# Kernel tuning notes

Hardware: AMD Instinct MI355X
Metric: run time of the kernel (lower is better)

## Reference

```python
import jax, jax.numpy as jnp
import numpy as np

B, S, D = 8, 8192, 512
E, DFF = 16, 512
CAPACITY = 2


def setup_inputs() -> dict:
    key = jax.random.key(0)
    ks = jax.random.split(key, 4)
    x = jax.random.normal(ks[0], (B, S, D), dtype=jnp.float32)
    gate_weight = jax.random.normal(ks[1], (D, E), dtype=jnp.float32) * 0.006
    w1 = jax.random.normal(ks[2], (E, D, DFF), dtype=jnp.float32) * 0.02
    b1 = jnp.zeros((E, DFF), dtype=jnp.float32)
    w2 = jax.random.normal(ks[3], (E, DFF, D), dtype=jnp.float32) * 0.02
    b2 = jnp.zeros((E, D), dtype=jnp.float32)
    return {"x": x, "gate_weight": gate_weight, "w1": w1, "b1": b1, "w2": w2, "b2": b2}


def reference(x, gate_weight, w1, b1, w2, b2):
    Bx, Sx, Dx = x.shape
    num_experts = gate_weight.shape[1]
    k = Sx // num_experts * CAPACITY  # tokens per expert (capacity limit)

    # Router: softmax over experts, then each expert picks its top-k tokens.
    logits = jnp.einsum('bsd,de->bse', x, gate_weight)
    affinity = jax.nn.softmax(logits, axis=-1).transpose(0, 2, 1)  # [b, e, s]
    gating, index = jax.lax.top_k(affinity, k)  # [b, e, k] each

    # Dispatch: gather selected tokens per expert (== one-hot einsum in torch).
    x_in = jnp.take_along_axis(x[:, None, :, :], index[..., None], axis=2)  # [b, e, k, d]

    # Per-expert MLP (grouped GEMM over expert axis).
    h = jax.nn.gelu(jnp.einsum('bekd,edh->bekh', x_in, w1) + b1[None, :, None, :])
    x_e = jnp.einsum('bekh,ehd->bekd', h, w2) + b2[None, :, None, :]

    # Combine: weight by gate prob and scatter-add back to token positions.
    weighted = gating[..., None] * x_e  # [b, e, k, d]
    out = jnp.zeros_like(x)
    idx_flat = index.reshape(Bx, num_experts * k)
    vals_flat = weighted.reshape(Bx, num_experts * k, Dx)
    out = out.at[jnp.arange(Bx)[:, None], idx_flat].add(vals_flat)
    return out
```

## Files before the change

kernel.cpp:

```cpp
#include <hip/hip_runtime.h>
#include <hip/hip_bf16.h>

typedef __attribute__((ext_vector_type(8))) short short8;
typedef __attribute__((ext_vector_type(4))) float floatx4;
typedef __attribute__((ext_vector_type(4))) unsigned short ushort4_t;

#define B_    8
#define S_    8192
#define D_    512
#define E_    16
#define DFF_  512
#define KROW_ 1024

__device__ __forceinline__ float bf2f(unsigned short u) {
    return __uint_as_float(((unsigned int)u) << 16);
}
__device__ __forceinline__ unsigned short f2bf(float f) {
    unsigned int u = __float_as_uint(f);
    u += 0x7FFFu + ((u >> 16) & 1u);
    return (unsigned short)(u >> 16);
}
__device__ __forceinline__ float gelu_tanh(float v) {
    const float t = 1.5957691216057308f * v * fmaf(0.044715f, v * v, 1.0f);
    return v * __builtin_amdgcn_rcpf(1.0f + __expf(-t));
}

#define GLD16(g, l) __builtin_amdgcn_global_load_lds( \
    (const __attribute__((address_space(1))) void*)(g), \
    (__attribute__((address_space(3))) void*)(l), 16, 0, 0)

__global__ __launch_bounds__(256) void cvt_x_k(
    const float* __restrict__ x, unsigned short* __restrict__ xb, int n4)
{
    int i = blockIdx.x * 256 + threadIdx.x;
    if (i >= n4) return;
    float4 v = ((const float4*)x)[i];
    ushort4_t o;
    o[0] = f2bf(v.x); o[1] = f2bf(v.y); o[2] = f2bf(v.z); o[3] = f2bf(v.w);
    ((ushort4_t*)xb)[i] = o;
}

__global__ __launch_bounds__(256) void transpose_w_k(
    const float* __restrict__ w1, const float* __restrict__ w2,
    unsigned short* __restrict__ w1t, unsigned short* __restrict__ w2t)
{
    __shared__ unsigned short tile[32][33];
    const int e = blockIdx.z & 15;
    const float*    src = (blockIdx.z < 16) ? w1 : w2;
    unsigned short* dst = (blockIdx.z < 16) ? w1t : w2t;
    const int x0 = blockIdx.x * 32, y0 = blockIdx.y * 32;
    const int tx = threadIdx.x, ty = threadIdx.y;
    const size_t base = (size_t)e * 512 * 512;
#pragma unroll
    for (int i = 0; i < 4; ++i)
        tile[ty + 8 * i][tx] = f2bf(src[base + (size_t)(y0 + ty + 8 * i) * 512 + x0 + tx]);
    __syncthreads();
#pragma unroll
    for (int i = 0; i < 4; ++i)
        dst[base + (size_t)(x0 + ty + 8 * i) * 512 + y0 + tx] = tile[tx][ty + 8 * i];
}

__global__ __launch_bounds__(256) void router_k(
    const float* __restrict__ x,
    const float* __restrict__ gw,
    float* __restrict__ aff)
{
    __shared__ float gws[D_ * E_];
    const int t = threadIdx.x;
    for (int i = t; i < D_ * E_; i += 256) gws[i] = gw[i];
    __syncthreads();

    const int tok = blockIdx.x * 256 + t;
    const float4* xr = (const float4*)(x + (size_t)tok * D_);
    float acc[E_];
#pragma unroll
    for (int e = 0; e < E_; ++e) acc[e] = 0.f;

    for (int d4 = 0; d4 < D_ / 4; ++d4) {
        float4 v = xr[d4];
#pragma unroll
        for (int q = 0; q < 4; ++q) {
            const float xv = (&v.x)[q];
            const float* g = &gws[(d4 * 4 + q) * E_];
#pragma unroll
            for (int e = 0; e < E_; ++e) acc[e] = fmaf(xv, g[e], acc[e]);
        }
    }
    float mx = acc[0];
#pragma unroll
    for (int e = 1; e < E_; ++e) mx = fmaxf(mx, acc[e]);
    float sm = 0.f;
#pragma unroll
    for (int e = 0; e < E_; ++e) { acc[e] = expf(acc[e] - mx); sm += acc[e]; }
    const float inv = 1.f / sm;
    const int b = tok >> 13, s = tok & (S_ - 1);
#pragma unroll
    for (int e = 0; e < E_; ++e)
        aff[((size_t)b * E_ + e) * S_ + s] = acc[e] * inv;
}

__global__ __launch_bounds__(1024) void topk_k(
    const float* __restrict__ aff, int* __restrict__ idxb, int* __restrict__ map)
{
    __shared__ unsigned int keys[S_];
    __shared__ unsigned int hist[4][257];
    __shared__ unsigned int sbuf[256];
    __shared__ unsigned int scan[1024];
    __shared__ unsigned int sh_b, sh_above, sh_ctr;

    const int b = blockIdx.x >> 4, e = blockIdx.x & 15;
    const float* a = aff + ((size_t)b * E_ + e) * S_;
    const int t = threadIdx.x;

    for (int i = t; i < S_; i += 1024) keys[i] = __float_as_uint(a[i]);
    if (t == 0) sh_ctr = 0;
    __syncthreads();

    unsigned int prefix = 0, need = KROW_;
#pragma unroll
    for (int lev = 0; lev < 4; ++lev) {
        const int shift = (lev == 0) ? 23 : (lev == 1) ? 15 : (lev == 2) ? 7 : 0;
        const int bins  = (lev == 3) ? 128 : 256;
        const unsigned int fmask = (unsigned int)(bins - 1);
        const int sw = shift + ((lev == 3) ? 7 : 8);
        const unsigned int mask_hi = 0xFFFFFFFFu << sw;

        hist[t >> 8][t & 255] = 0;
        __syncthreads();
        for (int i = t; i < S_; i += 1024) {
            unsigned int k = keys[i];
            if ((k & mask_hi) == prefix)
                atomicAdd(&hist[t >> 8][(k >> shift) & fmask], 1u);
        }
        __syncthreads();
        if (t < 256) sbuf[t] = hist[0][t] + hist[1][t] + hist[2][t] + hist[3][t];
        for (int off = 1; off < 256; off <<= 1) {
            __syncthreads();
            unsigned int v = 0;
            if (t < 256 && t + off < 256) v = sbuf[t + off];
            __syncthreads();
            if (t < 256) sbuf[t] += v;
        }
        __syncthreads();
        if (t < bins) {
            unsigned int c  = sbuf[t];
            unsigned int cn = (t + 1 < bins) ? sbuf[t + 1] : 0u;
            if (c >= need && cn < need) { sh_b = (unsigned int)t; sh_above = cn; }
        }
        __syncthreads();
        prefix |= sh_b << shift;
        need   -= sh_above;
        __syncthreads();
    }

    const unsigned int T = prefix;
    const unsigned int need_eq = need;
    const unsigned int m_gt = KROW_ - need_eq;

    int* idxg = idxb + ((size_t)b * E_ + e) * KROW_;
    for (int i = t; i < S_; i += 1024) {
        unsigned int k = keys[i];
        if (k > T) {
            unsigned int slot = atomicAdd(&sh_ctr, 1u);
            idxg[slot] = i;
            map[((size_t)b * S_ + i) * E_ + e] = (int)slot;
        }
    }
    unsigned int lt = 0;
    const int i0 = t * 8;
#pragma unroll
    for (int q = 0; q < 8; ++q) lt += (keys[i0 + q] == T);
    scan[t] = lt;
    for (int off = 1; off < 1024; off <<= 1) {
        __syncthreads();
        unsigned int v = (t >= off) ? scan[t - off] : 0u;
        __syncthreads();
        scan[t] += v;
    }
    __syncthreads();
    unsigned int r = scan[t] - lt;
#pragma unroll
    for (int q = 0; q < 8; ++q) {
        if (keys[i0 + q] == T) {
            if (r < need_eq) {
                idxg[m_gt + r] = i0 + q;
                map[((size_t)b * S_ + (i0 + q)) * E_ + e] = (int)(m_gt + r);
            }
            r++;
        }
    }
}

__global__ __launch_bounds__(256) void gemm1_k(
    const unsigned short* __restrict__ xb,
    const unsigned short* __restrict__ w1t,
    const float* __restrict__ b1,
    const int* __restrict__ idxb,
    unsigned short* __restrict__ h,
    int b_base)
{
    __shared__ unsigned short As[128 * 32];
    __shared__ unsigned short Bs[128 * 32];
    const int e  = blockIdx.z & 15;
    const int bl = blockIdx.z >> 4;
    const int b  = b_base + bl;
    const int m0 = blockIdx.x * 128;
    const int n0 = blockIdx.y * 128;
    const int t = threadIdx.x;
    const int w = t >> 6, l = t & 63;
    const int r0 = t >> 2, c0 = (t & 3) * 8;

    const int* idxg = idxb + ((size_t)b * E_ + e) * KROW_;
    const int s0 = idxg[m0 + r0];
    const int s1 = idxg[m0 + 64 + r0];
    const unsigned short* a0 = xb + ((size_t)b * S_ + s0) * D_ + c0;
    const unsigned short* a1 = xb + ((size_t)b * S_ + s1) * D_ + c0;
    const unsigned short* g0 = w1t + ((size_t)e * DFF_ + n0 + r0) * D_ + c0;
    const unsigned short* g1 = w1t + ((size_t)e * DFF_ + n0 + 64 + r0) * D_ + c0;
    unsigned short* asd = &As[w * 512];
    unsigned short* bsd = &Bs[w * 512];

    floatx4 acc[4][4];
#pragma unroll
    for (int i = 0; i < 4; ++i)
#pragma unroll
        for (int j = 0; j < 4; ++j) acc[i][j] = (floatx4){0.f, 0.f, 0.f, 0.f};

    const int wm = (w >> 1) * 64, wn = (w & 1) * 64;
    const int lane15 = l & 15, lk = (l >> 4) * 8;

    for (int k0 = 0; k0 < D_; k0 += 32) {
        __syncthreads();
        GLD16(a0 + k0, asd);
        GLD16(a1 + k0, asd + 2048);
        GLD16(g0 + k0, bsd);
        GLD16(g1 + k0, bsd + 2048);
        __syncthreads();
        short8 af[4], bf[4];
#pragma unroll
        for (int i = 0; i < 4; ++i) af[i] = *(const short8*)&As[(wm + i * 16 + lane15) * 32 + lk];
#pragma unroll
        for (int j = 0; j < 4; ++j) bf[j] = *(const short8*)&Bs[(wn + j * 16 + lane15) * 32 + lk];
#pragma unroll
        for (int i = 0; i < 4; ++i)
#pragma unroll
            for (int j = 0; j < 4; ++j)
                acc[i][j] = __builtin_amdgcn_mfma_f32_16x16x32_bf16(af[i], bf[j], acc[i][j], 0, 0, 0);
    }

    const size_t hbase = ((size_t)bl * E_ + e) * KROW_ * DFF_;
#pragma unroll
    for (int i = 0; i < 4; ++i)
#pragma unroll
        for (int j = 0; j < 4; ++j) {
            const int n = n0 + wn + j * 16 + lane15;
            const float bias = b1[e * DFF_ + n];
#pragma unroll
            for (int r = 0; r < 4; ++r) {
                const int m = m0 + wm + i * 16 + (l >> 4) * 4 + r;
                h[hbase + (size_t)m * DFF_ + n] = f2bf(gelu_tanh(acc[i][j][r] + bias));
            }
        }
}

__global__ __launch_bounds__(256) void gemm2_k(
    const unsigned short* __restrict__ h,
    const unsigned short* __restrict__ w2t,
    const float* __restrict__ b2,
    unsigned short* __restrict__ ex)
{
    __shared__ unsigned short As[128 * 32];
    __shared__ unsigned short Bs[128 * 32];
    const int e  = blockIdx.z & 15;
    const int bl = blockIdx.z >> 4;
    const int m0 = blockIdx.x * 128;
    const int n0 = blockIdx.y * 128;
    const int t = threadIdx.x;
    const int w = t >> 6, l = t & 63;
    const int r0 = t >> 2, c0 = (t & 3) * 8;

    const unsigned short* a0 = h + (((size_t)bl * E_ + e) * KROW_ + m0 + r0) * DFF_ + c0;
    const unsigned short* a1 = h + (((size_t)bl * E_ + e) * KROW_ + m0 + 64 + r0) * DFF_ + c0;
    const unsigned short* g0 = w2t + ((size_t)e * D_ + n0 + r0) * DFF_ + c0;
    const unsigned short* g1 = w2t + ((size_t)e * D_ + n0 + 64 + r0) * DFF_ + c0;
    unsigned short* asd = &As[w * 512];
    unsigned short* bsd = &Bs[w * 512];

    floatx4 acc[4][4];
#pragma unroll
    for (int i = 0; i < 4; ++i)
#pragma unroll
        for (int j = 0; j < 4; ++j) acc[i][j] = (floatx4){0.f, 0.f, 0.f, 0.f};

    const int wm = (w >> 1) * 64, wn = (w & 1) * 64;
    const int lane15 = l & 15, lk = (l >> 4) * 8;

    for (int k0 = 0; k0 < DFF_; k0 += 32) {
        __syncthreads();
        GLD16(a0 + k0, asd);
        GLD16(a1 + k0, asd + 2048);
        GLD16(g0 + k0, bsd);
        GLD16(g1 + k0, bsd + 2048);
        __syncthreads();
        short8 af[4], bf[4];
#pragma unroll
        for (int i = 0; i < 4; ++i) af[i] = *(const short8*)&As[(wm + i * 16 + lane15) * 32 + lk];
#pragma unroll
        for (int j = 0; j < 4; ++j) bf[j] = *(const short8*)&Bs[(wn + j * 16 + lane15) * 32 + lk];
#pragma unroll
        for (int i = 0; i < 4; ++i)
#pragma unroll
            for (int j = 0; j < 4; ++j)
                acc[i][j] = __builtin_amdgcn_mfma_f32_16x16x32_bf16(af[i], bf[j], acc[i][j], 0, 0, 0);
    }

    const size_t xbase = ((size_t)bl * E_ + e) * KROW_ * D_;
#pragma unroll
    for (int i = 0; i < 4; ++i)
#pragma unroll
        for (int j = 0; j < 4; ++j) {
            const int n = n0 + wn + j * 16 + lane15;
            const float bias = b2[e * D_ + n];
#pragma unroll
            for (int r = 0; r < 4; ++r) {
                const int m = m0 + wm + i * 16 + (l >> 4) * 4 + r;
                ex[xbase + (size_t)m * D_ + n] = f2bf(acc[i][j][r] + bias);
            }
        }
}

__global__ __launch_bounds__(256) void combine_k(
    const unsigned short* __restrict__ ex, const float* __restrict__ aff,
    const int* __restrict__ map, float* __restrict__ out, int b_base)
{
    const int t = threadIdx.x;
    const int w = t >> 6, l = t & 63;
    const size_t tokl = (size_t)blockIdx.x * 4 + w;
    const int bl = (int)(tokl >> 13);
    const int s  = (int)(tokl & (S_ - 1));
    const int b  = b_base + bl;

    int jv = -1; float gv = 0.f;
    if (l < 16) {
        jv = map[((size_t)b * S_ + s) * E_ + l];
        gv = aff[((size_t)b * E_ + l) * S_ + s];
    }
    float acc[8] = {0.f, 0.f, 0.f, 0.f, 0.f, 0.f, 0.f, 0.f};
#pragma unroll
    for (int e = 0; e < E_; ++e) {
        const int je = __shfl(jv, e);
        if (je < 0) continue;
        const float ge = __shfl(gv, e);
        const unsigned short* row = ex + (((size_t)bl * E_ + e) * KROW_ + je) * D_ + l * 8;
        short8 v = *(const short8*)row;
#pragma unroll
        for (int q = 0; q < 8; ++q) acc[q] += ge * bf2f((unsigned short)v[q]);
    }
    float* orow = out + ((size_t)b * S_ + s) * D_ + l * 8;
    float4 o0 = {acc[0], acc[1], acc[2], acc[3]};
    float4 o1 = {acc[4], acc[5], acc[6], acc[7]};
    ((float4*)orow)[0] = o0;
    ((float4*)orow)[1] = o1;
}

extern "C" void kernel_launch(void* const* d_in, const int* in_sizes, int n_in,
                              void* d_out, int out_size, void* d_ws, size_t ws_size,
                              hipStream_t stream) {
    const float* x  = (const float*)d_in[0];
    const float* gw = (const float*)d_in[1];
    const float* w1 = (const float*)d_in[2];
    const float* b1 = (const float*)d_in[3];
    const float* w2 = (const float*)d_in[4];
    const float* b2 = (const float*)d_in[5];
    float* out = (float*)d_out;
    char* ws = (char*)d_ws;

    size_t off = 0;
    float* aff = (float*)(ws + off);          off += (size_t)B_ * E_ * S_ * 4;
    int* idxb  = (int*)(ws + off);            off += (size_t)B_ * E_ * KROW_ * 4;
    int* map   = (int*)(ws + off);            off += (size_t)B_ * S_ * E_ * 4;
    unsigned short* w1t = (unsigned short*)(ws + off); off += (size_t)E_ * DFF_ * D_ * 2;
    unsigned short* w2t = (unsigned short*)(ws + off); off += (size_t)E_ * D_ * DFF_ * 2;
    unsigned short* xb  = (unsigned short*)(ws + off); off += (size_t)B_ * S_ * D_ * 2;
    const size_t fixed = off;
    const size_t per_b_h  = (size_t)E_ * KROW_ * DFF_ * 2;
    const size_t per_b_ex = (size_t)E_ * KROW_ * D_ * 2;
    const size_t per_b = per_b_h + per_b_ex;

    int bchunk = 1;
    if (ws_size > fixed + per_b) {
        size_t m = (ws_size - fixed) / per_b;
        bchunk = (int)(m > (size_t)B_ ? (size_t)B_ : m);
        if (bchunk < 1) bchunk = 1;
    }
    unsigned short* h  = (unsigned short*)(ws + fixed);
    unsigned short* ex = (unsigned short*)(ws + fixed + (size_t)bchunk * per_b_h);

    hipMemsetAsync(map, 0xFF, (size_t)B_ * S_ * E_ * 4, stream);
    cvt_x_k<<<dim3((B_ * S_ * D_ / 4 + 255) / 256), dim3(256), 0, stream>>>(
        x, xb, B_ * S_ * D_ / 4);
    transpose_w_k<<<dim3(16, 16, 32), dim3(32, 8, 1), 0, stream>>>(w1, w2, w1t, w2t);
    router_k<<<dim3((B_ * S_) / 256), dim3(256), 0, stream>>>(x, gw, aff);
    topk_k<<<dim3(B_ * E_), dim3(1024), 0, stream>>>(aff, idxb, map);

    for (int b0 = 0; b0 < B_; b0 += bchunk) {
        const int bc = (b0 + bchunk <= B_) ? bchunk : (B_ - b0);
        gemm1_k<<<dim3(KROW_ / 128, DFF_ / 128, bc * E_), dim3(256), 0, stream>>>(
            xb, w1t, b1, idxb, h, b0);
        gemm2_k<<<dim3(KROW_ / 128, D_ / 128, bc * E_), dim3(256), 0, stream>>>(
            h, w2t, b2, ex);
        combine_k<<<dim3(bc * (S_ / 4)), dim3(256), 0, stream>>>(ex, aff, map, out, b0);
    }
}
```

Before: 600.0 us.

## Double-buffer GEMM LDS tiles, fuse x bf16 conversion into router, hoist biases

Both expert GEMMs now use two LDS buffers, prefetching the next K-tile with async global-to-LDS loads while MFMAs run on the current one. This replaces two barriers per iteration with one and aims to hide load latency. The x-to-bf16 conversion moves into the router kernel, which already reads x, so one kernel launch and a full pass over x are dropped. Biases are loaded once before the epilogue and the GELU polynomial is refactored to save a multiply. The cost is twice the LDS per block, which can reduce occupancy, and the router now does strided per-thread bf16 writes that coalesce poorly.

Result: slower. 628.4 us (+4.7%).

```diff
diff --git a/kernel.cpp b/kernel.cpp
--- a/kernel.cpp
+++ b/kernel.cpp
@@ -21,24 +21,13 @@
     return (unsigned short)(u >> 16);
 }
 __device__ __forceinline__ float gelu_tanh(float v) {
-    const float t = 1.5957691216057308f * v * fmaf(0.044715f, v * v, 1.0f);
+    const float t = v * fmaf(0.0713548065f, v * v, 1.5957691216057308f);
     return v * __builtin_amdgcn_rcpf(1.0f + __expf(-t));
 }
 
 #define GLD16(g, l) __builtin_amdgcn_global_load_lds( \
     (const __attribute__((address_space(1))) void*)(g), \
     (__attribute__((address_space(3))) void*)(l), 16, 0, 0)
-
-__global__ __launch_bounds__(256) void cvt_x_k(
-    const float* __restrict__ x, unsigned short* __restrict__ xb, int n4)
-{
-    int i = blockIdx.x * 256 + threadIdx.x;
-    if (i >= n4) return;
-    float4 v = ((const float4*)x)[i];
-    ushort4_t o;
-    o[0] = f2bf(v.x); o[1] = f2bf(v.y); o[2] = f2bf(v.z); o[3] = f2bf(v.w);
-    ((ushort4_t*)xb)[i] = o;
-}
 
 __global__ __launch_bounds__(256) void transpose_w_k(
     const float* __restrict__ w1, const float* __restrict__ w2,
@@ -63,7 +52,8 @@
 __global__ __launch_bounds__(256) void router_k(
     const float* __restrict__ x,
     const float* __restrict__ gw,
-    float* __restrict__ aff)
+    float* __restrict__ aff,
+    unsigned short* __restrict__ xb)
 {
     __shared__ float gws[D_ * E_];
     const int t = threadIdx.x;
@@ -72,12 +62,16 @@
 
     const int tok = blockIdx.x * 256 + t;
     const float4* xr = (const float4*)(x + (size_t)tok * D_);
+    ushort4_t* xw = (ushort4_t*)(xb + (size_t)tok * D_);
     float acc[E_];
 #pragma unroll
     for (int e = 0; e < E_; ++e) acc[e] = 0.f;
 
     for (int d4 = 0; d4 < D_ / 4; ++d4) {
         float4 v = xr[d4];
+        ushort4_t o;
+        o[0] = f2bf(v.x); o[1] = f2bf(v.y); o[2] = f2bf(v.z); o[3] = f2bf(v.w);
+        xw[d4] = o;
 #pragma unroll
         for (int q = 0; q < 4; ++q) {
             const float xv = (&v.x)[q];
@@ -199,8 +193,8 @@
     unsigned short* __restrict__ h,
     int b_base)
 {
-    __shared__ unsigned short As[128 * 32];
-    __shared__ unsigned short Bs[128 * 32];
+    __shared__ unsigned short As[2][128 * 32];
+    __shared__ unsigned short Bs[2][128 * 32];
     const int e  = blockIdx.z & 15;
     const int bl = blockIdx.z >> 4;
     const int b  = b_base + bl;
@@ -217,8 +211,6 @@
     const unsigned short* a1 = xb + ((size_t)b * S_ + s1) * D_ + c0;
     const unsigned short* g0 = w1t + ((size_t)e * DFF_ + n0 + r0) * D_ + c0;
     const unsigned short* g1 = w1t + ((size_t)e * DFF_ + n0 + 64 + r0) * D_ + c0;
-    unsigned short* asd = &As[w * 512];
-    unsigned short* bsd = &Bs[w * 512];
 
     floatx4 acc[4][4];
 #pragma unroll
@@ -229,24 +221,40 @@
     const int wm = (w >> 1) * 64, wn = (w & 1) * 64;
     const int lane15 = l & 15, lk = (l >> 4) * 8;
 
-    for (int k0 = 0; k0 < D_; k0 += 32) {
-        __syncthreads();
-        GLD16(a0 + k0, asd);
-        GLD16(a1 + k0, asd + 2048);
-        GLD16(g0 + k0, bsd);
-        GLD16(g1 + k0, bsd + 2048);
-        __syncthreads();
+    {
+        unsigned short* asd = &As[0][w * 512];
+        unsigned short* bsd = &Bs[0][w * 512];
+        GLD16(a0, asd); GLD16(a1, asd + 2048);
+        GLD16(g0, bsd); GLD16(g1, bsd + 2048);
+    }
+    __syncthreads();
+
+#pragma unroll
+    for (int kt = 0; kt < D_ / 32; ++kt) {
+        const int cur = kt & 1;
+        if (kt + 1 < D_ / 32) {
+            const int k1 = (kt + 1) * 32;
+            unsigned short* asd = &As[cur ^ 1][w * 512];
+            unsigned short* bsd = &Bs[cur ^ 1][w * 512];
+            GLD16(a0 + k1, asd); GLD16(a1 + k1, asd + 2048);
+            GLD16(g0 + k1, bsd); GLD16(g1 + k1, bsd + 2048);
+        }
         short8 af[4], bf[4];
 #pragma unroll
-        for (int i = 0; i < 4; ++i) af[i] = *(const short8*)&As[(wm + i * 16 + lane15) * 32 + lk];
-#pragma unroll
-        for (int j = 0; j < 4; ++j) bf[j] = *(const short8*)&Bs[(wn + j * 16 + lane15) * 32 + lk];
+        for (int i = 0; i < 4; ++i) af[i] = *(const short8*)&As[cur][(wm + i * 16 + lane15) * 32 + lk];
+#pragma unroll
+        for (int j = 0; j < 4; ++j) bf[j] = *(const short8*)&Bs[cur][(wn + j * 16 + lane15) * 32 + lk];
 #pragma unroll
         for (int i = 0; i < 4; ++i)
 #pragma unroll
             for (int j = 0; j < 4; ++j)
                 acc[i][j] = __builtin_amdgcn_mfma_f32_16x16x32_bf16(af[i], bf[j], acc[i][j], 0, 0, 0);
-    }
+        __syncthreads();
+    }
+
+    float biasv[4];
+#pragma unroll
+    for (int j = 0; j < 4; ++j) biasv[j] = b1[e * DFF_ + n0 + wn + j * 16 + lane15];
 
     const size_t hbase = ((size_t)bl * E_ + e) * KROW_ * DFF_;
 #pragma unroll
@@ -254,11 +262,10 @@
 #pragma unroll
         for (int j = 0; j < 4; ++j) {
             const int n = n0 + wn + j * 16 + lane15;
-            const float bias = b1[e * DFF_ + n];
 #pragma unroll
             for (int r = 0; r < 4; ++r) {
                 const int m = m0 + wm + i * 16 + (l >> 4) * 4 + r;
-                h[hbase + (size_t)m * DFF_ + n] = f2bf(gelu_tanh(acc[i][j][r] + bias));
+                h[hbase + (size_t)m * DFF_ + n] = f2bf(gelu_tanh(acc[i][j][r] + biasv[j]));
             }
         }
 }
@@ -269,8 +276,8 @@
     const float* __restrict__ b2,
     unsigned short* __restrict__ ex)
 {
-    __shared__ unsigned short As[128 * 32];
-    __shared__ unsigned short Bs[128 * 32];
+    __shared__ unsigned short As[2][128 * 32];
+    __shared__ unsigned short Bs[2][128 * 32];
     const int e  = blockIdx.z & 15;
     const int bl = blockIdx.z >> 4;
     const int m0 = blockIdx.x * 128;
@@ -283,8 +290,6 @@
     const unsigned short* a1 = h + (((size_t)bl * E_ + e) * KROW_ + m0 + 64 + r0) * DFF_ + c0;
     const unsigned short* g0 = w2t + ((size_t)e * D_ + n0 + r0) * DFF_ + c0;
     const unsigned short* g1 = w2t + ((size_t)e * D_ + n0 + 64 + r0) * DFF_ + c0;
-    unsigned short* asd = &As[w * 512];
-    unsigned short* bsd = &Bs[w * 512];
 
     floatx4 acc[4][4];
 #pragma unroll
@@ -295,24 +300,40 @@
     const int wm = (w >> 1) * 64, wn = (w & 1) * 64;
     const int lane15 = l & 15, lk = (l >> 4) * 8;
 
-    for (int k0 = 0; k0 < DFF_; k0 += 32) {
-        __syncthreads();
-        GLD16(a0 + k0, asd);
-        GLD16(a1 + k0, asd + 2048);
-        GLD16(g0 + k0, bsd);
-        GLD16(g1 + k0, bsd + 2048);
-        __syncthreads();
+    {
+        unsigned short* asd = &As[0][w * 512];
+        unsigned short* bsd = &Bs[0][w * 512];
+        GLD16(a0, asd); GLD16(a1, asd + 2048);
+        GLD16(g0, bsd); GLD16(g1, bsd + 2048);
+    }
+    __syncthreads();
+
+#pragma unroll
+    for (int kt = 0; kt < DFF_ / 32; ++kt) {
+        const int cur = kt & 1;
+        if (kt + 1 < DFF_ / 32) {
+            const int k1 = (kt + 1) * 32;
+            unsigned short* asd = &As[cur ^ 1][w * 512];
+            unsigned short* bsd = &Bs[cur ^ 1][w * 512];
+            GLD16(a0 + k1, asd); GLD16(a1 + k1, asd + 2048);
+            GLD16(g0 + k1, bsd); GLD16(g1 + k1, bsd + 2048);
+        }
         short8 af[4], bf[4];
 #pragma unroll
-        for (int i = 0; i < 4; ++i) af[i] = *(const short8*)&As[(wm + i * 16 + lane15) * 32 + lk];
-#pragma unroll
-        for (int j = 0; j < 4; ++j) bf[j] = *(const short8*)&Bs[(wn + j * 16 + lane15) * 32 + lk];
+        for (int i = 0; i < 4; ++i) af[i] = *(const short8*)&As[cur][(wm + i * 16 + lane15) * 32 + lk];
+#pragma unroll
+        for (int j = 0; j < 4; ++j) bf[j] = *(const short8*)&Bs[cur][(wn + j * 16 + lane15) * 32 + lk];
 #pragma unroll
         for (int i = 0; i < 4; ++i)
 #pragma unroll
             for (int j = 0; j < 4; ++j)
                 acc[i][j] = __builtin_amdgcn_mfma_f32_16x16x32_bf16(af[i], bf[j], acc[i][j], 0, 0, 0);
-    }
+        __syncthreads();
+    }
+
+    float biasv[4];
+#pragma unroll
+    for (int j = 0; j < 4; ++j) biasv[j] = b2[e * D_ + n0 + wn + j * 16 + lane15];
 
     const size_t xbase = ((size_t)bl * E_ + e) * KROW_ * D_;
 #pragma unroll
@@ -320,11 +341,10 @@
 #pragma unroll
         for (int j = 0; j < 4; ++j) {
             const int n = n0 + wn + j * 16 + lane15;
-            const float bias = b2[e * D_ + n];
 #pragma unroll
             for (int r = 0; r < 4; ++r) {
                 const int m = m0 + wm + i * 16 + (l >> 4) * 4 + r;
-                ex[xbase + (size_t)m * D_ + n] = f2bf(acc[i][j][r] + bias);
+                ex[xbase + (size_t)m * D_ + n] = f2bf(acc[i][j][r] + biasv[j]);
             }
         }
 }
@@ -397,10 +417,8 @@
     unsigned short* ex = (unsigned short*)(ws + fixed + (size_t)bchunk * per_b_h);
 
     hipMemsetAsync(map, 0xFF, (size_t)B_ * S_ * E_ * 4, stream);
-    cvt_x_k<<<dim3((B_ * S_ * D_ / 4 + 255) / 256), dim3(256), 0, stream>>>(
-        x, xb, B_ * S_ * D_ / 4);
     transpose_w_k<<<dim3(16, 16, 32), dim3(32, 8, 1), 0, stream>>>(w1, w2, w1t, w2t);
-    router_k<<<dim3((B_ * S_) / 256), dim3(256), 0, stream>>>(x, gw, aff);
+    router_k<<<dim3((B_ * S_) / 256), dim3(256), 0, stream>>>(x, gw, aff, xb);
     topk_k<<<dim3(B_ * E_), dim3(1024), 0, stream>>>(aff, idxb, map);
 
     for (int b0 = 0; b0 < B_; b0 += bchunk) {
```
